# Optimization experiments

Hardware: AMD Instinct MI355X
Metric: run time of the kernel (lower is better)

Reference implementation:

```python
import jax, jax.numpy as jnp
import numpy as np

B, E, N, D = 32, 16384, 1000, 128


def setup_inputs() -> dict:
    key = jax.random.key(0)
    ks = jax.random.split(key, 8)
    s = 1.0 / np.sqrt(D)
    return {
        "edge_attr": jax.random.normal(ks[0], (B, E, D), dtype=jnp.float32),
        "edge_index": jax.random.randint(ks[1], (B, 2, E), 0, N, dtype=jnp.int32),
        "W1": jax.random.uniform(ks[2], (D, D), jnp.float32, -s, s),
        "b1": jax.random.uniform(ks[3], (D,), jnp.float32, -s, s),
        "W2": jax.random.uniform(ks[4], (D, D), jnp.float32, -s, s),
        "b2": jax.random.uniform(ks[5], (D,), jnp.float32, -s, s),
        "Wo": jax.random.uniform(ks[6], (1, D), jnp.float32, -s, s),
        "bo": jax.random.uniform(ks[7], (1,), jnp.float32, -s, s),
    }


def reference(edge_attr, edge_index, W1, b1, W2, b2, Wo, bo):
    # MLP over edge features: two hidden silu layers then sigmoid output * 10
    h = jax.nn.silu(jnp.einsum("bed,kd->bek", edge_attr, W1) + b1)
    h = jax.nn.silu(jnp.einsum("bed,kd->bek", h, W2) + b2)
    vals = jax.nn.sigmoid(jnp.einsum("bed,kd->bek", h, Wo) + bo)[..., 0] * 10.0  # [B, E]

    src = edge_index[:, 0, :]  # [B, E]
    dst = edge_index[:, 1, :]  # [B, E]
    b_idx = jnp.arange(B, dtype=edge_index.dtype)[:, None]  # [B, 1]
    heat = jnp.zeros((B, N, N), dtype=edge_attr.dtype).at[b_idx, src, dst].set(vals)

    # undirected_graph=True: symmetrize
    return (heat + jnp.swapaxes(heat, 1, 2)) * 0.5
```

## Files before the change

### kernel.cpp

```cpp
#include <hip/hip_runtime.h>
#include <hip/hip_bf16.h>
#include <math.h>

#define B_ 32
#define E_ 16384
#define N_ 1000
#define D_ 128
#define NN_ (N_ * N_)
#define T_ 4

typedef __attribute__((ext_vector_type(8))) short bf16x8;
typedef __attribute__((ext_vector_type(4))) float f32x4;

__device__ __forceinline__ unsigned short f2bf(float f) {
    unsigned u = __float_as_uint(f);
    u += 0x7FFFu + ((u >> 16) & 1u);
    return (unsigned short)(u >> 16);
}

__device__ __forceinline__ unsigned pk2(float lo, float hi) {
    __hip_bfloat162 h = __float22bfloat162_rn(make_float2(lo, hi));
    return *(unsigned*)&h;
}

__device__ __forceinline__ f32x4 mfma16(bf16x8 a, bf16x8 b, f32x4 c) {
    return __builtin_amdgcn_mfma_f32_16x16x32_bf16(a, b, c, 0, 0, 0);
}

__device__ __forceinline__ float silu_(float z) {
    return z * __builtin_amdgcn_rcpf(1.0f + __expf(-z));
}

__device__ __forceinline__ float decq(unsigned x) {
    return x ? (float)((x & 0x3FFFFu) - 1u) * (10.0f / 262142.0f) : 0.0f;
}

__device__ __forceinline__ void gload_lds16(const void* g, void* l) {
    __builtin_amdgcn_global_load_lds(
        (const __attribute__((address_space(1))) unsigned*)g,
        (__attribute__((address_space(3))) unsigned*)l, 16, 0, 0);
}

__global__ void prep_weights(const float* __restrict__ W1,
                             const float* __restrict__ W2,
                             unsigned short* __restrict__ wsz) {
    int t = blockIdx.x * 256 + threadIdx.x;
    int w = t >> 14, e = t & 16383;
    int row = e >> 7, col = e & 127;
    float v = (w ? W2 : W1)[e];
    char* dst = (char*)wsz + (size_t)w * 32768 + row * 256 + ((col * 2) ^ ((row & 7) << 4));
    *(unsigned short*)dst = f2bf(v);
}

__global__ __launch_bounds__(256, 2) void mlp_scatter_kernel(
    const float* __restrict__ X, const int* __restrict__ EI,
    const unsigned short* __restrict__ wsz,
    const float* __restrict__ b1, const float* __restrict__ b2,
    const float* __restrict__ Wo, const float* __restrict__ bo,
    unsigned* __restrict__ out)
{
    __shared__ __align__(16) char Wb[65536];
    __shared__ __align__(16) char Hs[8192];
    __shared__ __align__(16) float BiasL[384];

    const int tid = threadIdx.x;
    const int lane = tid & 63;
    const int wv = tid >> 6;
    const int l15 = lane & 15;
    const int g = (lane >> 4) & 3;
    char* hw = (char*)Hs + wv * 2048;

    const int bb = blockIdx.x >> 5;
    const int e0 = (blockIdx.x & 31) * (128 * T_);

    if (tid < 96) {
        const float* src = tid < 32 ? b1 : (tid < 64 ? b2 : Wo);
        ((f32x4*)BiasL)[tid] = ((const f32x4*)src)[tid & 31];
    }
    const float bo0 = bo[0];

    int eis[T_][2], eid[T_][2];
    #pragma unroll
    for (int st = 0; st < T_; ++st)
        #pragma unroll
        for (int m = 0; m < 2; ++m) {
            int e = e0 + st * 128 + wv * 32 + m * 16 + l15;
            eis[st][m] = EI[(size_t)bb * 2 * E_ + e];
            eid[st][m] = EI[(size_t)bb * 2 * E_ + E_ + e];
        }

    f32x4 af[2][4][2];

#define ISSUE_M(stv, mm) do {                                                        \
        unsigned long long _ad = (unsigned long long)X +                             \
            (((unsigned long long)((size_t)bb * E_ + e0 + (stv) * 128 + wv * 32 +    \
                                   (mm) * 16 + l15)) << 9) + (unsigned)(g * 32);     \
        asm volatile(                                                                \
            "global_load_dwordx4 %0, %8, off\n\t"                                    \
            "global_load_dwordx4 %1, %8, off offset:16\n\t"                          \
            "global_load_dwordx4 %2, %8, off offset:128\n\t"                         \
            "global_load_dwordx4 %3, %8, off offset:144\n\t"                         \
            "global_load_dwordx4 %4, %8, off offset:256\n\t"                         \
            "global_load_dwordx4 %5, %8, off offset:272\n\t"                         \
            "global_load_dwordx4 %6, %8, off offset:384\n\t"                         \
            "global_load_dwordx4 %7, %8, off offset:400"                             \
            : "=&v"(af[mm][0][0]), "=&v"(af[mm][0][1]), "=&v"(af[mm][1][0]),         \
              "=&v"(af[mm][1][1]), "=&v"(af[mm][2][0]), "=&v"(af[mm][2][1]),         \
              "=&v"(af[mm][3][0]), "=&v"(af[mm][3][1])                               \
            : "v"(_ad));                                                             \
    } while (0)

    ISSUE_M(0, 0);
    ISSUE_M(0, 1);

    #pragma unroll
    for (int it = 0; it < 16; ++it) {
        int off = it * 4096 + tid * 16;
        gload_lds16((const char*)wsz + off, Wb + off);
    }
    asm volatile("s_waitcnt vmcnt(0)" ::: "memory");
    __builtin_amdgcn_sched_barrier(0);
    __syncthreads();

    #pragma unroll
    for (int st = 0; st < T_; ++st) {
        asm volatile("s_waitcnt vmcnt(2)" ::: "memory");
        __builtin_amdgcn_sched_barrier(0);

        bf16x8 a[2][4];
        #pragma unroll
        for (int m = 0; m < 2; ++m)
            #pragma unroll
            for (int ks = 0; ks < 4; ++ks) {
                bf16x8 t;
                unsigned* tu = (unsigned*)&t;
                tu[0] = pk2(af[m][ks][0][0], af[m][ks][0][1]);
                tu[1] = pk2(af[m][ks][0][2], af[m][ks][0][3]);
                tu[2] = pk2(af[m][ks][1][0], af[m][ks][1][1]);
                tu[3] = pk2(af[m][ks][1][2], af[m][ks][1][3]);
                a[m][ks] = t;
            }

        f32x4 acc2[2][8];
        #pragma unroll
        for (int m = 0; m < 2; ++m)
            #pragma unroll
            for (int n = 0; n < 8; ++n)
                acc2[m][n] = (f32x4){0.f, 0.f, 0.f, 0.f};

        #pragma unroll
        for (int q = 0; q < 4; ++q) {
            f32x4 acc1[2][2];
            #pragma unroll
            for (int m = 0; m < 2; ++m)
                #pragma unroll
                for (int nn = 0; nn < 2; ++nn)
                    acc1[m][nn] = (f32x4){0.f, 0.f, 0.f, 0.f};

            #pragma unroll
            for (int ks = 0; ks < 4; ++ks)
                #pragma unroll
                for (int nn = 0; nn < 2; ++nn) {
                    int row = l15 + (q * 2 + nn) * 16;
                    bf16x8 aw = *(const bf16x8*)(Wb + row * 256 +
                                  ((ks * 64 + g * 16) ^ ((row & 7) << 4)));
                    acc1[0][nn] = mfma16(aw, a[0][ks], acc1[0][nn]);
                    acc1[1][nn] = mfma16(aw, a[1][ks], acc1[1][nn]);
                }

            #pragma unroll
            for (int nn = 0; nn < 2; ++nn) {
                f32x4 b1q = ((f32x4*)BiasL)[(q * 2 + nn) * 4 + g];
                #pragma unroll
                for (int m = 0; m < 2; ++m) {
                    float h0 = silu_(acc1[m][nn][0] + b1q[0]);
                    float h1 = silu_(acc1[m][nn][1] + b1q[1]);
                    float h2 = silu_(acc1[m][nn][2] + b1q[2]);
                    float h3 = silu_(acc1[m][nn][3] + b1q[3]);
                    int edge = m * 16 + l15;
                    *(uint2*)(hw + edge * 64 + ((nn * 32 + g * 8) ^ ((edge & 6) << 3))) =
                        make_uint2(pk2(h0, h1), pk2(h2, h3));
                }
            }

            if (st + 1 < T_ && q == 2) ISSUE_M(st + 1, 0);

            bf16x8 hb[2];
            #pragma unroll
            for (int m = 0; m < 2; ++m) {
                int edge = m * 16 + l15;
                hb[m] = *(const bf16x8*)(hw + edge * 64 + ((g * 16) ^ ((edge & 6) << 3)));
            }
            #pragma unroll
            for (int n = 0; n < 8; ++n) {
                int row = l15 + n * 16;
                bf16x8 w2 = *(const bf16x8*)(Wb + 32768 + row * 256 +
                              ((q * 64 + g * 16) ^ ((row & 7) << 4)));
                acc2[0][n] = mfma16(w2, hb[0], acc2[0][n]);
                acc2[1][n] = mfma16(w2, hb[1], acc2[1][n]);
            }
        }

        float zed[2] = {0.f, 0.f};
        #pragma unroll
        for (int n = 0; n < 8; ++n) {
            f32x4 b2q = ((f32x4*)BiasL)[32 + n * 4 + g];
            f32x4 woq = ((f32x4*)BiasL)[64 + n * 4 + g];
            #pragma unroll
            for (int m = 0; m < 2; ++m) {
                zed[m] += silu_(acc2[m][n][0] + b2q[0]) * woq[0];
                zed[m] += silu_(acc2[m][n][1] + b2q[1]) * woq[1];
                zed[m] += silu_(acc2[m][n][2] + b2q[2]) * woq[2];
                zed[m] += silu_(acc2[m][n][3] + b2q[3]) * woq[3];
            }
        }

        if (st + 1 < T_) ISSUE_M(st + 1, 1);

        #pragma unroll
        for (int m = 0; m < 2; ++m) {
            zed[m] += __shfl_xor(zed[m], 16, 64);
            zed[m] += __shfl_xor(zed[m], 32, 64);
        }

        if (g == 0) {
            #pragma unroll
            for (int m = 0; m < 2; ++m) {
                int e = e0 + st * 128 + wv * 32 + m * 16 + l15;
                float z = zed[m] + bo0;
                float val = 10.0f * __builtin_amdgcn_rcpf(1.0f + __expf(-z));
                unsigned qv = (unsigned)(val * 26214.2f + 0.5f) + 1u;
                if (qv > 0x3FFFFu) qv = 0x3FFFFu;
                unsigned packed = ((unsigned)e << 18) | qv;
                unsigned long long aaddr = (unsigned long long)(out +
                    ((size_t)bb * NN_ + (size_t)eis[st][m] * N_ + eid[st][m]));
                asm volatile("global_atomic_umax %0, %1, off"
                             :: "v"(aaddr), "v"(packed) : "memory");
            }
        }
    }
#undef ISSUE_M
}

__global__ __launch_bounds__(256) void finalize1(
    const int* __restrict__ EI, const unsigned* __restrict__ out,
    float* __restrict__ ev)
{
    int i = blockIdx.x * 256 + threadIdx.x;
    int b = i >> 14, e = i & 16383;
    int s = EI[(size_t)b * 2 * E_ + e];
    int d = EI[(size_t)b * 2 * E_ + E_ + e];
    const unsigned* ob = out + (size_t)b * NN_;
    ev[i] = 0.5f * (decq(ob[(size_t)s * N_ + d]) + decq(ob[(size_t)d * N_ + s]));
}

__global__ __launch_bounds__(256) void finalize2(
    const int* __restrict__ EI, const float* __restrict__ ev,
    float* __restrict__ outf)
{
    int i = blockIdx.x * 256 + threadIdx.x;
    int b = i >> 14, e = i & 16383;
    int s = EI[(size_t)b * 2 * E_ + e];
    int d = EI[(size_t)b * 2 * E_ + E_ + e];
    float v = ev[i];
    float* ob = outf + (size_t)b * NN_;
    ob[(size_t)s * N_ + d] = v;
    ob[(size_t)d * N_ + s] = v;
}

__global__ __launch_bounds__(256) void symmetrize_kernel(unsigned* __restrict__ out) {
    const int b = blockIdx.y;
    const int ti = blockIdx.x >> 5;
    const int tj = blockIdx.x & 31;
    if (ti > tj) return;
    __shared__ unsigned ta[32][33];
    __shared__ unsigned tb[32][33];
    const int j = threadIdx.x & 31;
    const int i0 = threadIdx.x >> 5;
    unsigned* ob = out + (size_t)b * NN_;
    float* of = (float*)ob;
    #pragma unroll
    for (int rr = 0; rr < 4; ++rr) {
        int i = rr * 8 + i0;
        int gi = ti * 32 + i, gj = tj * 32 + j;
        ta[i][j] = (gi < N_ && gj < N_) ? ob[(size_t)gi * N_ + gj] : 0u;
        int hi = tj * 32 + i, hj = ti * 32 + j;
        tb[i][j] = (hi < N_ && hj < N_) ? ob[(size_t)hi * N_ + hj] : 0u;
    }
    __syncthreads();
    #pragma unroll
    for (int rr = 0; rr < 4; ++rr) {
        int i = rr * 8 + i0;
        int gi = ti * 32 + i, gj = tj * 32 + j;
        if (gi < N_ && gj < N_)
            of[(size_t)gi * N_ + gj] = 0.5f * (decq(ta[i][j]) + decq(tb[j][i]));
        int hi = tj * 32 + i, hj = ti * 32 + j;
        if (hi < N_ && hj < N_)
            of[(size_t)hi * N_ + hj] = 0.5f * (decq(tb[i][j]) + decq(ta[j][i]));
    }
}

extern "C" void kernel_launch(void* const* d_in, const int* in_sizes, int n_in,
                              void* d_out, int out_size, void* d_ws, size_t ws_size,
                              hipStream_t stream) {
    const float* X  = (const float*)d_in[0];
    const int*   EI = (const int*)d_in[1];
    const float* W1 = (const float*)d_in[2];
    const float* b1 = (const float*)d_in[3];
    const float* W2 = (const float*)d_in[4];
    const float* b2 = (const float*)d_in[5];
    const float* Wo = (const float*)d_in[6];
    const float* bo = (const float*)d_in[7];
    unsigned* out = (unsigned*)d_out;
    unsigned short* wsz = (unsigned short*)d_ws;
    float* ev = (float*)((char*)d_ws + 65536);

    prep_weights<<<dim3(128), dim3(256), 0, stream>>>(W1, W2, wsz);
    hipMemsetAsync(d_out, 0, (size_t)B_ * NN_ * sizeof(float), stream);
    mlp_scatter_kernel<<<dim3((B_ * E_) / (128 * T_)), dim3(256), 0, stream>>>(
        X, EI, wsz, b1, b2, Wo, bo, out);

    if (ws_size >= 65536 + (size_t)B_ * E_ * sizeof(float)) {
        finalize1<<<dim3((B_ * E_) / 256), dim3(256), 0, stream>>>(EI, out, ev);
        finalize2<<<dim3((B_ * E_) / 256), dim3(256), 0, stream>>>(EI, ev, (float*)d_out);
    } else {
        symmetrize_kernel<<<dim3(32 * 32, B_), dim3(256), 0, stream>>>(out);
    }
}
```

Measured before the change: 144.3 us.

## Fuse finalize passes into one in-place kernel with tagged quantized encoding

The two finalize kernels and their intermediate edge-value buffer are replaced by one kernel that symmetrizes in place. Slots still holding a raw max-atomic result are marked by a high tag bit, and slots already rewritten as positive floats are reused directly, so concurrent in-place rewrites stay consistent. To free that tag bit, the quantization drops to 17 bits. Separately, both next-stage prefetches are now issued at the start of each stage instead of being spread through the compute loop. This trades output precision and register pressure for one fewer launch and less global memory traffic.

```diff
diff --git a/kernel.cpp b/kernel.cpp
--- a/kernel.cpp
+++ b/kernel.cpp
@@ -31,8 +31,8 @@
     return z * __builtin_amdgcn_rcpf(1.0f + __expf(-z));
 }
 
-__device__ __forceinline__ float decq(unsigned x) {
-    return x ? (float)((x & 0x3FFFFu) - 1u) * (10.0f / 262142.0f) : 0.0f;
+__device__ __forceinline__ float dec17(unsigned x) {
+    return (float)((x & 0x1FFFFu) - 1u) * (10.0f / 131070.0f);
 }
 
 __device__ __forceinline__ void gload_lds16(const void* g, void* l) {
@@ -141,6 +141,8 @@
                 a[m][ks] = t;
             }
 
+        if (st + 1 < T_) { ISSUE_M(st + 1, 0); ISSUE_M(st + 1, 1); }
+
         f32x4 acc2[2][8];
         #pragma unroll
         for (int m = 0; m < 2; ++m)
@@ -183,8 +185,6 @@
                 }
             }
 
-            if (st + 1 < T_ && q == 2) ISSUE_M(st + 1, 0);
-
             bf16x8 hb[2];
             #pragma unroll
             for (int m = 0; m < 2; ++m) {
@@ -215,8 +215,6 @@
             }
         }
 
-        if (st + 1 < T_) ISSUE_M(st + 1, 1);
-
         #pragma unroll
         for (int m = 0; m < 2; ++m) {
             zed[m] += __shfl_xor(zed[m], 16, 64);
@@ -229,9 +227,9 @@
                 int e = e0 + st * 128 + wv * 32 + m * 16 + l15;
                 float z = zed[m] + bo0;
                 float val = 10.0f * __builtin_amdgcn_rcpf(1.0f + __expf(-z));
-                unsigned qv = (unsigned)(val * 26214.2f + 0.5f) + 1u;
-                if (qv > 0x3FFFFu) qv = 0x3FFFFu;
-                unsigned packed = ((unsigned)e << 18) | qv;
+                unsigned qv = (unsigned)(val * 13107.0f + 0.5f) + 1u;
+                if (qv > 0x1FFFFu) qv = 0x1FFFFu;
+                unsigned packed = 0x80000000u | ((unsigned)e << 17) | qv;
                 unsigned long long aaddr = (unsigned long long)(out +
                     ((size_t)bb * NN_ + (size_t)eis[st][m] * N_ + eid[st][m]));
                 asm volatile("global_atomic_umax %0, %1, off"
@@ -242,62 +240,27 @@
 #undef ISSUE_M
 }
 
-__global__ __launch_bounds__(256) void finalize1(
-    const int* __restrict__ EI, const unsigned* __restrict__ out,
-    float* __restrict__ ev)
+__global__ __launch_bounds__(256) void finalize_fused(
+    const int* __restrict__ EI, unsigned* __restrict__ out)
 {
     int i = blockIdx.x * 256 + threadIdx.x;
     int b = i >> 14, e = i & 16383;
     int s = EI[(size_t)b * 2 * E_ + e];
     int d = EI[(size_t)b * 2 * E_ + E_ + e];
-    const unsigned* ob = out + (size_t)b * NN_;
-    ev[i] = 0.5f * (decq(ob[(size_t)s * N_ + d]) + decq(ob[(size_t)d * N_ + s]));
-}
-
-__global__ __launch_bounds__(256) void finalize2(
-    const int* __restrict__ EI, const float* __restrict__ ev,
-    float* __restrict__ outf)
-{
-    int i = blockIdx.x * 256 + threadIdx.x;
-    int b = i >> 14, e = i & 16383;
-    int s = EI[(size_t)b * 2 * E_ + e];
-    int d = EI[(size_t)b * 2 * E_ + E_ + e];
-    float v = ev[i];
-    float* ob = outf + (size_t)b * NN_;
-    ob[(size_t)s * N_ + d] = v;
-    ob[(size_t)d * N_ + s] = v;
-}
-
-__global__ __launch_bounds__(256) void symmetrize_kernel(unsigned* __restrict__ out) {
-    const int b = blockIdx.y;
-    const int ti = blockIdx.x >> 5;
-    const int tj = blockIdx.x & 31;
-    if (ti > tj) return;
-    __shared__ unsigned ta[32][33];
-    __shared__ unsigned tb[32][33];
-    const int j = threadIdx.x & 31;
-    const int i0 = threadIdx.x >> 5;
     unsigned* ob = out + (size_t)b * NN_;
-    float* of = (float*)ob;
-    #pragma unroll
-    for (int rr = 0; rr < 4; ++rr) {
-        int i = rr * 8 + i0;
-        int gi = ti * 32 + i, gj = tj * 32 + j;
-        ta[i][j] = (gi < N_ && gj < N_) ? ob[(size_t)gi * N_ + gj] : 0u;
-        int hi = tj * 32 + i, hj = ti * 32 + j;
-        tb[i][j] = (hi < N_ && hj < N_) ? ob[(size_t)hi * N_ + hj] : 0u;
-    }
-    __syncthreads();
-    #pragma unroll
-    for (int rr = 0; rr < 4; ++rr) {
-        int i = rr * 8 + i0;
-        int gi = ti * 32 + i, gj = tj * 32 + j;
-        if (gi < N_ && gj < N_)
-            of[(size_t)gi * N_ + gj] = 0.5f * (decq(ta[i][j]) + decq(tb[j][i]));
-        int hi = tj * 32 + i, hj = ti * 32 + j;
-        if (hi < N_ && hj < N_)
-            of[(size_t)hi * N_ + hj] = 0.5f * (decq(tb[i][j]) + decq(ta[j][i]));
-    }
+    unsigned x1 = ob[(size_t)s * N_ + d];
+    unsigned x2 = ob[(size_t)d * N_ + s];
+    float v;
+    if (!(x1 >> 31) && x1)      v = __uint_as_float(x1);
+    else if (!(x2 >> 31) && x2) v = __uint_as_float(x2);
+    else {
+        float c1 = (x1 >> 31) ? dec17(x1) : 0.0f;
+        float c2 = (x2 >> 31) ? dec17(x2) : 0.0f;
+        v = 0.5f * (c1 + c2);
+    }
+    unsigned uv = __float_as_uint(v);
+    ob[(size_t)s * N_ + d] = uv;
+    ob[(size_t)d * N_ + s] = uv;
 }
 
 extern "C" void kernel_launch(void* const* d_in, const int* in_sizes, int n_in,
@@ -313,17 +276,10 @@
     const float* bo = (const float*)d_in[7];
     unsigned* out = (unsigned*)d_out;
     unsigned short* wsz = (unsigned short*)d_ws;
-    float* ev = (float*)((char*)d_ws + 65536);
 
     prep_weights<<<dim3(128), dim3(256), 0, stream>>>(W1, W2, wsz);
     hipMemsetAsync(d_out, 0, (size_t)B_ * NN_ * sizeof(float), stream);
     mlp_scatter_kernel<<<dim3((B_ * E_) / (128 * T_)), dim3(256), 0, stream>>>(
         X, EI, wsz, b1, b2, Wo, bo, out);
-
-    if (ws_size >= 65536 + (size_t)B_ * E_ * sizeof(float)) {
-        finalize1<<<dim3((B_ * E_) / 256), dim3(256), 0, stream>>>(EI, out, ev);
-        finalize2<<<dim3((B_ * E_) / 256), dim3(256), 0, stream>>>(EI, ev, (float*)d_out);
-    } else {
-        symmetrize_kernel<<<dim3(32 * 32, B_), dim3(256), 0, stream>>>(out);
-    }
-}
+    finalize_fused<<<dim3((B_ * E_) / 256), dim3(256), 0, stream>>>(EI, out);
+}
```

Measured after the change: 145.6 us. No clear change (+0.9%).
